# Optimization experiments

Measured on AMD Instinct MI355X. Metric: run time of the kernel, lower is better.

## Reference

```python
import jax, jax.numpy as jnp
import numpy as np

B, N, E, H, HID = 4, 2048, 1024, 16, 4096
D = E // H
EPS = 1e-5


def setup_inputs() -> dict:
    key = jax.random.key(0)
    ks = jax.random.split(key, 8)
    s = 0.02
    return {
        "x": jax.random.normal(ks[0], (B, N, E), dtype=jnp.float32),
        "Wqkv": jax.random.normal(ks[1], (3 * E, E), dtype=jnp.float32) * s,
        "bqkv": jnp.zeros((3 * E,), dtype=jnp.float32),
        "Wo": jax.random.normal(ks[2], (E, E), dtype=jnp.float32) * s,
        "bo": jnp.zeros((E,), dtype=jnp.float32),
        "ln1_g": jnp.ones((E,), dtype=jnp.float32),
        "ln1_b": jnp.zeros((E,), dtype=jnp.float32),
        "W1": jax.random.normal(ks[3], (HID, E), dtype=jnp.float32) * s,
        "bf1": jnp.zeros((HID,), dtype=jnp.float32),
        "W2": jax.random.normal(ks[4], (E, HID), dtype=jnp.float32) * s,
        "bf2": jnp.zeros((E,), dtype=jnp.float32),
        "ln2_g": jnp.ones((E,), dtype=jnp.float32),
        "ln2_b": jnp.zeros((E,), dtype=jnp.float32),
    }


def _layernorm(x, g, b):
    m = jnp.mean(x, axis=-1, keepdims=True)
    v = jnp.mean(jnp.square(x - m), axis=-1, keepdims=True)
    return (x - m) * jax.lax.rsqrt(v + EPS) * g + b


def reference(x, Wqkv, bqkv, Wo, bo, ln1_g, ln1_b, W1, bf1, W2, bf2, ln2_g, ln2_b):
    Bx, Nx, Ex = x.shape
    # --- MultiHeadSelfAttention (faithful to original, including its einsum-label quirk) ---
    qkv = x @ Wqkv.T + bqkv                                   # (B,N,3E)
    qkv = qkv.reshape(Bx, Nx, 3, H, D).transpose(2, 0, 3, 1, 4)  # (3,B,H,N,D)
    q, k, v = qkv[0], qkv[1], qkv[2]                          # each (B,H,N,D)
    # original torch labels: q/k interpreted as (n,q,h,d) -> energy (B,N,H,H)
    energy = jnp.einsum('nqhd,nkhd->nhqk', q, k)
    attention = jax.nn.softmax(energy / (Ex ** 0.5), axis=-1)  # softmax over heads axis
    out = jnp.einsum('nhql,nlhd->nqhd', attention, v).reshape(Bx, Nx, Ex)
    attn_out = out @ Wo.T + bo
    # --- residual + LN1 ---
    h = _layernorm(x + attn_out, ln1_g, ln1_b)
    # --- FFN (dropout is identity in eval) ---
    f = jax.nn.gelu(h @ W1.T + bf1, approximate=False) @ W2.T + bf2
    # --- residual + LN2 ---
    return _layernorm(h + f, ln2_g, ln2_b)
```

## Files before the change

kernel.cpp:

```cpp
#include <hip/hip_runtime.h>
#include <hip/hip_bf16.h>
#include <math.h>

typedef __hip_bfloat16 bf16;
typedef __bf16 bf8v __attribute__((ext_vector_type(8)));
typedef float f4v __attribute__((ext_vector_type(4)));

__device__ inline void storeC(bf16* p, float v) { *p = __float2bfloat16(v); }
__device__ inline void storeC(float* p, float v) { *p = v; }

__device__ inline void gld16(const void* g, void* l) {
    __builtin_amdgcn_global_load_lds(
        (__attribute__((address_space(1))) void*)g,
        (__attribute__((address_space(3))) void*)l, 16, 0, 0);
}

__global__ __launch_bounds__(256)
void cast_f2b(const float* __restrict__ X, bf16* __restrict__ Y, long n)
{
    const long i = ((long)blockIdx.x * 256 + threadIdx.x) * 4;
    if (i + 3 < n) {
        const float4 v = *(const float4*)(X + i);
        Y[i + 0] = __float2bfloat16(v.x);
        Y[i + 1] = __float2bfloat16(v.y);
        Y[i + 2] = __float2bfloat16(v.z);
        Y[i + 3] = __float2bfloat16(v.w);
    }
}

template<int ACT, bool HASRES, typename CT, int K, int BN>
__global__ __launch_bounds__(512, 2)
void gemm256(const bf16* __restrict__ A, const bf16* __restrict__ W,
             const float* __restrict__ bias, const float* __restrict__ Rr,
             CT* __restrict__ C, int N)
{
    extern __shared__ __align__(16) unsigned short lds[];
    constexpr int NT   = K / 32;
    constexpr int NREP = BN / 64;
    constexpr int A_SH = 256 * 32;
    constexpr int SLOT = A_SH + BN * 32;

    int id = blockIdx.y * gridDim.x + blockIdx.x;
    const int nwg = gridDim.x * gridDim.y;
    id = (id & 7) * (nwg >> 3) + (id >> 3);
    const int bm = id % gridDim.x;
    const int bn = id / gridDim.x;
    const long row0 = (long)bm * 256;
    const long col0 = (long)bn * BN;

    const int tid  = threadIdx.x;
    const int lane = tid & 63;
    const int wave = tid >> 6;
    const int wm = wave >> 2;
    const int wn = wave & 3;
    const int fr = lane & 15;
    const int ksw = (((lane >> 4) ^ ((lane >> 2) & 3)) << 3);

    const int srow = tid >> 2;
    const int csrc = (tid & 3) ^ ((srow >> 2) & 3);
    const unsigned short* gA = (const unsigned short*)A + (row0 + srow) * (long)K + csrc * 8;
    const unsigned short* gB = (const unsigned short*)W + (col0 + srow) * (long)K + csrc * 8;
    unsigned short* const wbase = lds + wave * 512;

    auto stage = [&](int t) {
        const long k0 = (long)t * 32;
        unsigned short* sl = wbase + (t & 3) * SLOT;
        gld16(gA + k0,                 sl);
        gld16(gA + 128 * (long)K + k0, sl + 4096);
        gld16(gB + k0,                 sl + A_SH);
        if constexpr (BN == 256)
            gld16(gB + 128 * (long)K + k0, sl + A_SH + 4096);
    };

    f4v acc[8][NREP];
#pragma unroll
    for (int i = 0; i < 8; ++i)
#pragma unroll
        for (int j = 0; j < NREP; ++j) acc[i][j] = {0.f, 0.f, 0.f, 0.f};

    stage(0); stage(1); stage(2);

#pragma unroll 4
    for (int t = 0; t < NT; ++t) {
        if constexpr (BN == 256) {
            if (t + 2 < NT)      asm volatile("s_waitcnt vmcnt(8)" ::: "memory");
            else if (t + 1 < NT) asm volatile("s_waitcnt vmcnt(4)" ::: "memory");
            else                 asm volatile("s_waitcnt vmcnt(0)" ::: "memory");
        } else {
            if (t + 2 < NT)      asm volatile("s_waitcnt vmcnt(6)" ::: "memory");
            else if (t + 1 < NT) asm volatile("s_waitcnt vmcnt(3)" ::: "memory");
            else                 asm volatile("s_waitcnt vmcnt(0)" ::: "memory");
        }
        __builtin_amdgcn_s_barrier();
        __builtin_amdgcn_sched_barrier(0);
        if (t + 3 < NT) stage(t + 3);

        const unsigned short* sA = lds + (t & 3) * SLOT;
        const unsigned short* sB = sA + A_SH;

        bf8v bfrag[NREP];
#pragma unroll
        for (int ni = 0; ni < NREP; ++ni)
            bfrag[ni] = *(const bf8v*)&sB[(wn * (NREP * 16) + ni * 16 + fr) * 32 + ksw];

#pragma unroll
        for (int ph = 0; ph < 2; ++ph) {
            bf8v afrag[4];
#pragma unroll
            for (int mi = 0; mi < 4; ++mi)
                afrag[mi] = *(const bf8v*)&sA[(wm * 128 + ph * 64 + mi * 16 + fr) * 32 + ksw];
            __builtin_amdgcn_s_setprio(1);
#pragma unroll
            for (int mi = 0; mi < 4; ++mi)
#pragma unroll
                for (int ni = 0; ni < NREP; ++ni)
                    acc[ph * 4 + mi][ni] = __builtin_amdgcn_mfma_f32_16x16x32_bf16(
                        afrag[mi], bfrag[ni], acc[ph * 4 + mi][ni], 0, 0, 0);
            __builtin_amdgcn_s_setprio(0);
        }
    }
    __builtin_amdgcn_sched_barrier(0);

#pragma unroll
    for (int ni = 0; ni < NREP; ++ni) {
        const long n = col0 + wn * (NREP * 16) + ni * 16 + fr;
        const float bvv = bias[n];
#pragma unroll
        for (int mi = 0; mi < 8; ++mi) {
            const long mbase = row0 + wm * 128 + mi * 16 + (lane >> 4) * 4;
#pragma unroll
            for (int r = 0; r < 4; ++r) {
                float v0 = acc[mi][ni][r] + bvv;
                if (HASRES) v0 += Rr[(mbase + r) * (long)N + n];
                if (ACT == 1) v0 = 0.5f * v0 * (1.f + erff(v0 * 0.70710678118654752f));
                storeC(&C[(mbase + r) * (long)N + n], v0);
            }
        }
    }
}

__global__ __launch_bounds__(256)
void attn_kernel(const bf16* __restrict__ qkv, bf16* __restrict__ scr)
{
    __shared__ float sb[4][3392];
    const int tid = threadIdx.x;
    const int wave = tid >> 6, lane = tid & 63;
    const int m = blockIdx.x * 4 + wave;

    float* q = sb[wave];
    float* k = q + 1040;
    float* v = k + 1040;
    float* a = v + 1040;

    const bf16* rowp = qkv + (size_t)m * 3072;
    for (int i = lane; i < 1024; i += 64) {
        int hh = i >> 6, dd = i & 63;
        q[hh * 65 + dd] = __bfloat162float(rowp[i]);
        k[hh * 65 + dd] = __bfloat162float(rowp[1024 + i]);
        v[hh * 65 + dd] = __bfloat162float(rowp[2048 + i]);
    }
    __syncthreads();

    const int h1 = lane & 15, qd = lane >> 4;
    float e[4];
#pragma unroll
    for (int j = 0; j < 4; ++j) {
        const float* qr = q + h1 * 65;
        const float* kr = k + (qd * 4 + j) * 65;
        float s0 = 0.f;
        for (int d = 0; d < 64; ++d) s0 += qr[d] * kr[d];
        e[j] = s0 * 0.03125f;
    }
    float mx = fmaxf(fmaxf(e[0], e[1]), fmaxf(e[2], e[3]));
    mx = fmaxf(mx, __shfl_xor(mx, 16, 64));
    mx = fmaxf(mx, __shfl_xor(mx, 32, 64));
    float p[4], ps = 0.f;
#pragma unroll
    for (int j = 0; j < 4; ++j) { p[j] = expf(e[j] - mx); ps += p[j]; }
    ps += __shfl_xor(ps, 16, 64);
    ps += __shfl_xor(ps, 32, 64);
    const float inv = 1.f / ps;
#pragma unroll
    for (int j = 0; j < 4; ++j) a[h1 * 17 + qd * 4 + j] = p[j] * inv;
    __syncthreads();

    const int h = lane & 15, dg = lane >> 4;
    float arow[16];
#pragma unroll
    for (int l2 = 0; l2 < 16; ++l2) arow[l2] = a[h * 17 + l2];
    const int b = m >> 11, j = m & 2047;
    bf16* op = scr + (((size_t)b * 2048 + h * 128 + (j >> 4)) * 1024 + (j & 15) * 64);
    for (int t = 0; t < 16; ++t) {
        const int d = dg * 16 + t;
        float o = 0.f;
#pragma unroll
        for (int l2 = 0; l2 < 16; ++l2) o += arow[l2] * v[l2 * 65 + d];
        op[d] = __float2bfloat16(o);
    }
}

__global__ __launch_bounds__(256)
void ln_kernel(const float* __restrict__ X, const float* __restrict__ G,
               const float* __restrict__ Bt, float* __restrict__ Y32,
               bf16* __restrict__ Yb)
{
    __shared__ float rs[4], rq[4];
    const int tid = threadIdx.x;
    const long row = blockIdx.x;
    const float* xp = X + row * 1024;
    float x[4];
#pragma unroll
    for (int i = 0; i < 4; ++i) x[i] = xp[tid + 256 * i];

    float s = x[0] + x[1] + x[2] + x[3];
#pragma unroll
    for (int off = 32; off; off >>= 1) s += __shfl_down(s, off, 64);
    if ((tid & 63) == 0) rs[tid >> 6] = s;
    __syncthreads();
    const float mean = (rs[0] + rs[1] + rs[2] + rs[3]) * (1.f / 1024.f);

    float qv = 0.f;
#pragma unroll
    for (int i = 0; i < 4; ++i) { float d = x[i] - mean; qv += d * d; }
#pragma unroll
    for (int off = 32; off; off >>= 1) qv += __shfl_down(qv, off, 64);
    if ((tid & 63) == 0) rq[tid >> 6] = qv;
    __syncthreads();
    const float var = (rq[0] + rq[1] + rq[2] + rq[3]) * (1.f / 1024.f);
    const float rstd = rsqrtf(var + 1e-5f);

#pragma unroll
    for (int i = 0; i < 4; ++i) {
        const int e = tid + 256 * i;
        const float yv = (x[i] - mean) * rstd * G[e] + Bt[e];
        Y32[row * 1024 + e] = yv;
        if (Yb) Yb[row * 1024 + e] = __float2bfloat16(yv);
    }
}

extern "C" void kernel_launch(void* const* d_in, const int* in_sizes, int n_in,
                              void* d_out, int out_size, void* d_ws, size_t ws_size,
                              hipStream_t stream)
{
    (void)in_sizes; (void)n_in; (void)out_size;
    const float* x    = (const float*)d_in[0];
    const float* Wqkv = (const float*)d_in[1];
    const float* bqkv = (const float*)d_in[2];
    const float* Wo   = (const float*)d_in[3];
    const float* bo   = (const float*)d_in[4];
    const float* g1   = (const float*)d_in[5];
    const float* b1   = (const float*)d_in[6];
    const float* W1   = (const float*)d_in[7];
    const float* bf1  = (const float*)d_in[8];
    const float* W2   = (const float*)d_in[9];
    const float* bf2  = (const float*)d_in[10];
    const float* g2   = (const float*)d_in[11];
    const float* b2   = (const float*)d_in[12];
    float* out = (float*)d_out;

    if (ws_size < 125829120ULL) return;

    char* ws = (char*)d_ws;
    bf16* qkv   = (bf16*)(ws + 0);
    float* t    = (float*)(ws + 0);
    bf16* u     = (bf16*)(ws + 0);
    bf16* Wqkvb = (bf16*)(ws + 67108864);
    bf16* Wob   = (bf16*)(ws + 73400320);
    bf16* W1b   = (bf16*)(ws + 75497472);
    bf16* W2b   = (bf16*)(ws + 83886080);
    bf16* xb    = (bf16*)(ws + 92274688);
    bf16* scr   = (bf16*)(ws + 92274688);
    bf16* hb    = (bf16*)(ws + 109051904);
    float* h    = out;

    cast_f2b<<<8192, 256, 0, stream>>>(x,    xb,    8388608);
    cast_f2b<<<3072, 256, 0, stream>>>(Wqkv, Wqkvb, 3145728);
    cast_f2b<<<1024, 256, 0, stream>>>(Wo,   Wob,   1048576);
    cast_f2b<<<4096, 256, 0, stream>>>(W1,   W1b,   4194304);
    cast_f2b<<<4096, 256, 0, stream>>>(W2,   W2b,   4194304);

    gemm256<0, false, bf16, 1024, 256><<<dim3(32, 12), 512, 131072, stream>>>(xb, Wqkvb, bqkv, nullptr, qkv, 3072);
    attn_kernel<<<2048, 256, 0, stream>>>(qkv, scr);
    gemm256<0, true, float, 1024, 128><<<dim3(32, 8), 512, 98304, stream>>>(scr, Wob, bo, x, t, 1024);
    ln_kernel<<<8192, 256, 0, stream>>>(t, g1, b1, h, hb);
    gemm256<1, false, bf16, 1024, 256><<<dim3(32, 16), 512, 131072, stream>>>(hb, W1b, bf1, nullptr, u, 4096);
    gemm256<0, true, float, 4096, 128><<<dim3(32, 8), 512, 98304, stream>>>(u, W2b, bf2, h, out, 1024);
    ln_kernel<<<8192, 256, 0, stream>>>(out, g2, b2, out, nullptr);
}
```

Before: 532.9 us.

## Stage GEMM epilogue through LDS for vectorized coalesced stores and remap tiles

The GEMM epilogue now writes the accumulators into padded LDS in two halves, then reads them back row-contiguously. Bias, residual, GELU and output stores all become 4-wide vector accesses instead of scattered scalar ones. The block-to-tile mapping also changes so that groups of 8 blocks cover 4 adjacent row tiles, aiming for better L2 reuse. The BN=256 GEMMs need more LDS, which may affect occupancy, and the epilogue adds extra barriers.

```diff
diff --git a/kernel.cpp b/kernel.cpp
--- a/kernel.cpp
+++ b/kernel.cpp
@@ -6,8 +6,9 @@
 typedef __bf16 bf8v __attribute__((ext_vector_type(8)));
 typedef float f4v __attribute__((ext_vector_type(4)));
 
-__device__ inline void storeC(bf16* p, float v) { *p = __float2bfloat16(v); }
-__device__ inline void storeC(float* p, float v) { *p = v; }
+__device__ inline float gelu_act(float v) {
+    return 0.5f * v * (1.f + erff(v * 0.70710678118654752f));
+}
 
 __device__ inline void gld16(const void* g, void* l) {
     __builtin_amdgcn_global_load_lds(
@@ -40,11 +41,10 @@
     constexpr int A_SH = 256 * 32;
     constexpr int SLOT = A_SH + BN * 32;
 
-    int id = blockIdx.y * gridDim.x + blockIdx.x;
-    const int nwg = gridDim.x * gridDim.y;
-    id = (id & 7) * (nwg >> 3) + (id >> 3);
-    const int bm = id % gridDim.x;
-    const int bn = id / gridDim.x;
+    const int o     = blockIdx.y * gridDim.x + blockIdx.x;
+    const int local = o >> 3;
+    const int bm = (o & 7) * 4 + (local & 3);
+    const int bn = local >> 2;
     const long row0 = (long)bm * 256;
     const long col0 = (long)bn * BN;
 
@@ -121,19 +121,57 @@
     }
     __builtin_amdgcn_sched_barrier(0);
 
-#pragma unroll
-    for (int ni = 0; ni < NREP; ++ni) {
-        const long n = col0 + wn * (NREP * 16) + ni * 16 + fr;
-        const float bvv = bias[n];
-#pragma unroll
-        for (int mi = 0; mi < 8; ++mi) {
-            const long mbase = row0 + wm * 128 + mi * 16 + (lane >> 4) * 4;
-#pragma unroll
-            for (int r = 0; r < 4; ++r) {
-                float v0 = acc[mi][ni][r] + bvv;
-                if (HASRES) v0 += Rr[(mbase + r) * (long)N + n];
-                if (ACT == 1) v0 = 0.5f * v0 * (1.f + erff(v0 * 0.70710678118654752f));
-                storeC(&C[(mbase + r) * (long)N + n], v0);
+    constexpr int STR = (BN == 256) ? 260 : 132;
+    constexpr int LPR = BN / 4;
+    constexpr int RPI = 64 / LPR;
+    float* eb = (float*)lds;
+    const int q4    = (lane >> 4) * 4;
+    const int wrcol = wn * (NREP * 16) + fr;
+    const int lcol  = (lane % LPR) * 4;
+    const int lrow  = lane / LPR;
+    const long nbase = col0 + lcol;
+    const float4 b4 = *(const float4*)&bias[nbase];
+    const float bb[4] = {b4.x, b4.y, b4.z, b4.w};
+
+#pragma unroll
+    for (int h = 0; h < 2; ++h) {
+        __syncthreads();
+        if (wm == h) {
+#pragma unroll
+            for (int mi = 0; mi < 8; ++mi)
+#pragma unroll
+                for (int ni = 0; ni < NREP; ++ni)
+#pragma unroll
+                    for (int r = 0; r < 4; ++r)
+                        eb[(mi * 16 + q4 + r) * STR + wrcol + ni * 16] = acc[mi][ni][r];
+        }
+        __syncthreads();
+#pragma unroll
+        for (int i = 0; i < 16 / RPI; ++i) {
+            const int  rh = wave * 16 + i * RPI + lrow;
+            const long gr = row0 + h * 128 + rh;
+            const f4v v = *(const f4v*)&eb[rh * STR + lcol];
+            float ov[4];
+#pragma unroll
+            for (int c = 0; c < 4; ++c) ov[c] = v[c] + bb[c];
+            if (HASRES) {
+                const float4 r4 = *(const float4*)&Rr[gr * (long)N + nbase];
+                const float ra[4] = {r4.x, r4.y, r4.z, r4.w};
+#pragma unroll
+                for (int c = 0; c < 4; ++c) ov[c] += ra[c];
+            }
+            if (ACT == 1) {
+#pragma unroll
+                for (int c = 0; c < 4; ++c) ov[c] = gelu_act(ov[c]);
+            }
+            if constexpr (sizeof(CT) == 2) {
+                ushort4 s;
+                bf16* sp = (bf16*)&s;
+#pragma unroll
+                for (int c = 0; c < 4; ++c) sp[c] = __float2bfloat16(ov[c]);
+                *(ushort4*)&C[gr * (long)N + nbase] = s;
+            } else {
+                *(float4*)&C[gr * (long)N + nbase] = make_float4(ov[0], ov[1], ov[2], ov[3]);
             }
         }
     }
@@ -273,17 +311,20 @@
     bf16* hb    = (bf16*)(ws + 109051904);
     float* h    = out;
 
+    constexpr unsigned LDS_BIG   = 133120;
+    constexpr unsigned LDS_SMALL = 98304;
+
     cast_f2b<<<8192, 256, 0, stream>>>(x,    xb,    8388608);
     cast_f2b<<<3072, 256, 0, stream>>>(Wqkv, Wqkvb, 3145728);
     cast_f2b<<<1024, 256, 0, stream>>>(Wo,   Wob,   1048576);
     cast_f2b<<<4096, 256, 0, stream>>>(W1,   W1b,   4194304);
     cast_f2b<<<4096, 256, 0, stream>>>(W2,   W2b,   4194304);
 
-    gemm256<0, false, bf16, 1024, 256><<<dim3(32, 12), 512, 131072, stream>>>(xb, Wqkvb, bqkv, nullptr, qkv, 3072);
+    gemm256<0, false, bf16, 1024, 256><<<dim3(32, 12), 512, LDS_BIG, stream>>>(xb, Wqkvb, bqkv, nullptr, qkv, 3072);
     attn_kernel<<<2048, 256, 0, stream>>>(qkv, scr);
-    gemm256<0, true, float, 1024, 128><<<dim3(32, 8), 512, 98304, stream>>>(scr, Wob, bo, x, t, 1024);
+    gemm256<0, true, float, 1024, 128><<<dim3(32, 8), 512, LDS_SMALL, stream>>>(scr, Wob, bo, x, t, 1024);
     ln_kernel<<<8192, 256, 0, stream>>>(t, g1, b1, h, hb);
-    gemm256<1, false, bf16, 1024, 256><<<dim3(32, 16), 512, 131072, stream>>>(hb, W1b, bf1, nullptr, u, 4096);
-    gemm256<0, true, float, 4096, 128><<<dim3(32, 8), 512, 98304, stream>>>(u, W2b, bf2, h, out, 1024);
+    gemm256<1, false, bf16, 1024, 256><<<dim3(32, 16), 512, LDS_BIG, stream>>>(hb, W1b, bf1, nullptr, u, 4096);
+    gemm256<0, true, float, 4096, 128><<<dim3(32, 8), 512, LDS_SMALL, stream>>>(u, W2b, bf2, h, out, 1024);
     ln_kernel<<<8192, 256, 0, stream>>>(out, g2, b2, out, nullptr);
 }
```

After: 471.0 us. 11.6% less time.
